# Kernel optimization log

Measured on AMD Instinct MI355X. Metric: run time of the kernel, lower is better.

## Reference

```python
import jax, jax.numpy as jnp
import numpy as np

B, S, M_DIM, N_DIM, K_NNZ = 8, 2048, 2048, 2048, 205


def setup_inputs() -> dict:
    key = jax.random.key(0)
    k1, k2, k3, k4 = jax.random.split(key, 4)
    x = jax.random.normal(k1, (B, S, M_DIM), dtype=jnp.float32)
    # CSR structure: K_NNZ unique, sorted column indices per row
    scores = jax.random.uniform(k2, (N_DIM, M_DIM))
    cols = jnp.sort(jnp.argsort(scores, axis=1)[:, :K_NNZ], axis=1)  # [N, K] unique per row
    indices = cols.reshape(-1).astype(jnp.int32)                      # [nnz]
    indptr = (jnp.arange(N_DIM + 1) * K_NNZ).astype(jnp.int32)        # [N+1]
    W_val = jax.random.normal(k3, (N_DIM * K_NNZ,), dtype=jnp.float32) * (1.0 / np.sqrt(M_DIM))
    bias = jax.random.normal(k4, (N_DIM,), dtype=jnp.float32) * 0.01
    return {"x": x, "W_val": W_val, "bias": bias, "indices": indices, "indptr": indptr}


def reference(x, W_val, bias, indices, indptr):
    # SparseLinear.forward: y = x @ W^T + bias, with W stored in CSR
    # (W_val: nnz values, indptr: [N+1] row pointers, indices: [nnz] column ids).
    N = indptr.shape[0] - 1
    M = x.shape[-1]
    nnz = W_val.shape[0]
    # row id of each nonzero, derived from indptr (standard CSR expansion)
    row_ids = jnp.searchsorted(indptr, jnp.arange(nnz, dtype=indptr.dtype), side="right") - 1
    # materialize the sparse weight (CSR columns are unique per row -> set is exact)
    W = jnp.zeros((N, M), dtype=W_val.dtype).at[row_ids, indices].set(W_val)
    return jnp.einsum("bsm,nm->bsn", x, W) + bias
```

## Files before the change

kernel.cpp:

```cpp
#include <hip/hip_runtime.h>
#include <hip/hip_bf16.h>
#include <stdint.h>

#define M_TOT 16384
#define K_TOT 2048
#define N_TOT 2048

#define BM 256
#define BN 256
#define BK 64
#define LDS_HALF (128 * 64)

#define W_BLOCKS 2048
#define CAST_BLOCKS 16384

typedef __attribute__((ext_vector_type(8))) short short8;
typedef __attribute__((ext_vector_type(4))) float float4v;
typedef __attribute__((ext_vector_type(8))) unsigned short ushort8;

__device__ __forceinline__ unsigned short f2bf_rne(float f) {
    union { float f; unsigned u; } a; a.f = f;
    unsigned r = a.u + 0x7FFFu + ((a.u >> 16) & 1u);
    return (unsigned short)(r >> 16);
}

__global__ void prep_kernel(const float* __restrict__ x,
                            const float* __restrict__ val, const int* __restrict__ idx,
                            const int* __restrict__ indptr,
                            unsigned short* __restrict__ xb, unsigned short* __restrict__ Wb) {
    const int b = blockIdx.x;
    if (b < W_BLOCKS) {
        const int n = b;
        unsigned short* row = Wb + (size_t)n * K_TOT;
        ushort8 z = {0, 0, 0, 0, 0, 0, 0, 0};
        ((ushort8*)row)[threadIdx.x] = z;
        __syncthreads();
        const int s = indptr[n], e = indptr[n + 1];
        for (int j = s + (int)threadIdx.x; j < e; j += (int)blockDim.x)
            row[idx[j]] = f2bf_rne(val[j]);
    } else {
        const int i = (b - W_BLOCKS) * 256 + (int)threadIdx.x;
        const float4* xf = (const float4*)x;
        float4 a = xf[2 * i];
        float4 c = xf[2 * i + 1];
        ushort8 o;
        o[0] = f2bf_rne(a.x); o[1] = f2bf_rne(a.y); o[2] = f2bf_rne(a.z); o[3] = f2bf_rne(a.w);
        o[4] = f2bf_rne(c.x); o[5] = f2bf_rne(c.y); o[6] = f2bf_rne(c.z); o[7] = f2bf_rne(c.w);
        ((ushort8*)xb)[i] = o;
    }
}

__global__ __launch_bounds__(512, 2) void gemm_bias_kernel_256(
    const unsigned short* __restrict__ A,
    const unsigned short* __restrict__ Bw,
    const float* __restrict__ bias,
    float* __restrict__ C)
{
    extern __shared__ unsigned short lds[];

    const int tid  = threadIdx.x;
    const int lane = tid & 63;
    const int wave = tid >> 6;

    const int raw = blockIdx.x;
    const int lid = (raw & 7) * 64 + (raw >> 3);
    const int bm = lid >> 3;
    const int bn = lid & 7;

    const int wrow = wave >> 2;
    const int wcol = wave & 3;
    const int wr16 = wrow * 16;
    const int wc16 = wcol * 16;
    const int mrow = lane & 15;
    const int quad = lane >> 4;
    const int rx   = mrow & 7;

    const int srow = lane >> 3;
    const int csrc = ((lane & 7) ^ srow) * 8;
    const unsigned short* pA = A  + (size_t)(bm * BM + wave * 8 + srow) * K_TOT + csrc;
    const unsigned short* pB = Bw + (size_t)(bn * BN + wave * 8 + srow) * K_TOT + csrc;
    unsigned short* lw = lds + wave * 8 * 64;

    float4v acc[8][4] = {};

#define STAGE(PG, MATIDX, BUF, H, K0)                                            \
    { _Pragma("unroll")                                                          \
      for (int l = 0; l < 2; ++l) {                                              \
        const unsigned short* g = (PG) + ((size_t)((H) * 128 + l * 64) * K_TOT + (size_t)(K0)); \
        unsigned short* lp = lw + (((BUF) * 4 + (MATIDX) * 2 + (H)) * LDS_HALF) + l * 64 * 64;  \
        __builtin_amdgcn_global_load_lds(                                        \
            (const __attribute__((address_space(1))) unsigned int*)g,            \
            (__attribute__((address_space(3))) unsigned int*)lp, 16, 0, 0);      \
      } }

#define WAITV4 asm volatile("s_waitcnt vmcnt(4)" ::: "memory")
#define WAITV0 asm volatile("s_waitcnt vmcnt(0)" ::: "memory")
#define NOSTG  ((void)0)
#define NOWT   ((void)0)

#define PHASE(BUF, MH, NH, STG, TAILW)                                           \
  {                                                                              \
    const unsigned short* Ah = lds + ((BUF) * 4 + (MH)) * LDS_HALF;              \
    const unsigned short* Bh = lds + ((BUF) * 4 + 2 + (NH)) * LDS_HALF;          \
    short8 af[4][2], bfr[2][2];                                                  \
    _Pragma("unroll")                                                            \
    for (int mi = 0; mi < 4; ++mi) {                                             \
      const int r = mi * 32 + wr16 + mrow;                                       \
      _Pragma("unroll")                                                          \
      for (int ks = 0; ks < 2; ++ks)                                             \
        af[mi][ks] = *(const short8*)(Ah + r * 64 + (((ks * 4 + quad) ^ rx) * 8)); \
    }                                                                            \
    _Pragma("unroll")                                                            \
    for (int ni = 0; ni < 2; ++ni) {                                             \
      const int r = ni * 64 + wc16 + mrow;                                       \
      _Pragma("unroll")                                                          \
      for (int ks = 0; ks < 2; ++ks)                                             \
        bfr[ni][ks] = *(const short8*)(Bh + r * 64 + (((ks * 4 + quad) ^ rx) * 8)); \
    }                                                                            \
    STG;                                                                         \
    asm volatile("" ::: "memory");                                               \
    __builtin_amdgcn_s_barrier();                                                \
    asm volatile("s_waitcnt lgkmcnt(0)" ::: "memory");                           \
    __builtin_amdgcn_s_setprio(1);                                               \
    _Pragma("unroll")                                                            \
    for (int mi = 0; mi < 4; ++mi)                                               \
      _Pragma("unroll")                                                          \
      for (int ni = 0; ni < 2; ++ni)                                             \
        _Pragma("unroll")                                                        \
        for (int ks = 0; ks < 2; ++ks)                                           \
          acc[(MH) * 4 + mi][(NH) * 2 + ni] =                                    \
              __builtin_amdgcn_mfma_f32_16x16x32_bf16(                           \
                  af[mi][ks], bfr[ni][ks], acc[(MH) * 4 + mi][(NH) * 2 + ni], 0, 0, 0); \
    __builtin_amdgcn_s_setprio(0);                                               \
    TAILW;                                                                       \
    asm volatile("" ::: "memory");                                               \
    __builtin_amdgcn_s_barrier();                                                \
    asm volatile("" ::: "memory");                                               \
  }

    STAGE(pA, 0, 0, 0, 0);
    STAGE(pB, 1, 0, 1, 0);
    STAGE(pB, 1, 0, 0, 0);
    STAGE(pA, 0, 0, 1, 0);
    STAGE(pA, 0, 1, 0, 64);
    STAGE(pB, 1, 1, 1, 64);
    WAITV4;
    asm volatile("" ::: "memory");
    __builtin_amdgcn_s_barrier();
    asm volatile("" ::: "memory");

    int k0b = 64, k0c = 128, k0d = 192;
#pragma unroll 1
    for (int it = 0; it < 15; ++it) {
        PHASE(0, 0, 0, STAGE(pB, 1, 1, 0, k0b), NOWT)
        PHASE(0, 0, 1, STAGE(pA, 0, 1, 1, k0b), NOWT)
        PHASE(0, 1, 1, STAGE(pA, 0, 0, 0, k0c), NOWT)
        PHASE(0, 1, 0, STAGE(pB, 1, 0, 1, k0c), WAITV4)
        PHASE(1, 0, 0, STAGE(pB, 1, 0, 0, k0c), NOWT)
        PHASE(1, 0, 1, STAGE(pA, 0, 0, 1, k0c), NOWT)
        PHASE(1, 1, 1, STAGE(pA, 0, 1, 0, k0d), NOWT)
        PHASE(1, 1, 0, STAGE(pB, 1, 1, 1, k0d), WAITV4)
        k0b += 128; k0c += 128; k0d += 128;
    }
    PHASE(0, 0, 0, STAGE(pB, 1, 1, 0, k0b), NOWT)
    PHASE(0, 0, 1, STAGE(pA, 0, 1, 1, k0b), NOWT)
    PHASE(0, 1, 1, NOSTG, NOWT)
    PHASE(0, 1, 0, NOSTG, WAITV0)
    PHASE(1, 0, 0, NOSTG, NOWT)
    PHASE(1, 0, 1, NOSTG, NOWT)
    PHASE(1, 1, 1, NOSTG, NOWT)
    PHASE(1, 1, 0, NOSTG, NOWT)

#pragma unroll
    for (int nh = 0; nh < 2; ++nh)
#pragma unroll
        for (int ni = 0; ni < 2; ++ni) {
            const int col = bn * BN + nh * 128 + ni * 64 + wc16 + mrow;
            const float bv = bias[col];
#pragma unroll
            for (int mh = 0; mh < 2; ++mh)
#pragma unroll
                for (int mi = 0; mi < 4; ++mi) {
                    const int row0 = bm * BM + mh * 128 + mi * 32 + wr16 + quad * 4;
#pragma unroll
                    for (int r = 0; r < 4; ++r)
                        C[(size_t)(row0 + r) * N_TOT + col] =
                            acc[mh * 4 + mi][nh * 2 + ni][r] + bv;
                }
        }
#undef PHASE
#undef STAGE
#undef WAITV4
#undef WAITV0
#undef NOSTG
#undef NOWT
}

#define FBM 128
#define FBN 128
#define FBK 64
__global__ __launch_bounds__(256) void gemm_bias_kernel_128(
    const unsigned short* __restrict__ A,
    const unsigned short* __restrict__ Bw,
    const float* __restrict__ bias,
    float* __restrict__ C)
{
    __shared__ unsigned short Asm[FBM * FBK];
    __shared__ unsigned short Bsm[FBN * FBK];

    const int tid  = threadIdx.x;
    const int lane = tid & 63;
    const int wave = tid >> 6;
    const int bm = blockIdx.y;
    const int bn = blockIdx.x;

    const int srow_l = lane >> 3;
    const int schunk = ((lane & 7) ^ srow_l) * 8;
    const unsigned short* a_g[4];
    const unsigned short* b_g[4];
    unsigned short* a_l[4];
    unsigned short* b_l[4];
#pragma unroll
    for (int l = 0; l < 4; ++l) {
        const int row = wave * 32 + l * 8 + srow_l;
        a_g[l] = A  + (size_t)(bm * FBM + row) * K_TOT + schunk;
        b_g[l] = Bw + (size_t)(bn * FBN + row) * K_TOT + schunk;
        a_l[l] = Asm + (wave * 32 + l * 8) * FBK;
        b_l[l] = Bsm + (wave * 32 + l * 8) * FBK;
    }

    const int wm = (wave >> 1) * 64;
    const int wn = (wave & 1) * 64;
    const int mrow = lane & 15;
    const int quad = lane >> 4;
    const int rx   = mrow & 7;

    float4v acc[4][4] = {};

    for (int k0 = 0; k0 < K_TOT; k0 += FBK) {
        __syncthreads();
#pragma unroll
        for (int l = 0; l < 4; ++l)
            __builtin_amdgcn_global_load_lds(
                (const __attribute__((address_space(1))) unsigned int*)(a_g[l] + k0),
                (__attribute__((address_space(3))) unsigned int*)a_l[l], 16, 0, 0);
#pragma unroll
        for (int l = 0; l < 4; ++l)
            __builtin_amdgcn_global_load_lds(
                (const __attribute__((address_space(1))) unsigned int*)(b_g[l] + k0),
                (__attribute__((address_space(3))) unsigned int*)b_l[l], 16, 0, 0);
        __syncthreads();

#pragma unroll
        for (int ks = 0; ks < 2; ++ks) {
            short8 af[4], bf_[4];
#pragma unroll
            for (int mi = 0; mi < 4; ++mi) {
                const int r = wm + mi * 16 + mrow;
                const int slot = (ks * 4 + quad) ^ rx;
                af[mi] = *(const short8*)(Asm + r * FBK + slot * 8);
            }
#pragma unroll
            for (int ni = 0; ni < 4; ++ni) {
                const int r = wn + ni * 16 + mrow;
                const int slot = (ks * 4 + quad) ^ rx;
                bf_[ni] = *(const short8*)(Bsm + r * FBK + slot * 8);
            }
#pragma unroll
            for (int mi = 0; mi < 4; ++mi)
#pragma unroll
                for (int ni = 0; ni < 4; ++ni)
                    acc[mi][ni] = __builtin_amdgcn_mfma_f32_16x16x32_bf16(
                        af[mi], bf_[ni], acc[mi][ni], 0, 0, 0);
        }
    }

#pragma unroll
    for (int ni = 0; ni < 4; ++ni) {
        const int col = bn * FBN + wn + ni * 16 + mrow;
        const float bv = bias[col];
#pragma unroll
        for (int mi = 0; mi < 4; ++mi) {
#pragma unroll
            for (int r = 0; r < 4; ++r) {
                const int row = bm * FBM + wm + mi * 16 + quad * 4 + r;
                C[(size_t)row * N_TOT + col] = acc[mi][ni][r] + bv;
            }
        }
    }
}

extern "C" void kernel_launch(void* const* d_in, const int* in_sizes, int n_in,
                              void* d_out, int out_size, void* d_ws, size_t ws_size,
                              hipStream_t stream) {
    const float* x       = (const float*)d_in[0];
    const float* W_val   = (const float*)d_in[1];
    const float* bias    = (const float*)d_in[2];
    const int*   indices = (const int*)d_in[3];
    const int*   indptr  = (const int*)d_in[4];
    float* out = (float*)d_out;

    unsigned short* xb = (unsigned short*)d_ws;
    unsigned short* Wb = xb + (size_t)M_TOT * K_TOT;
    if (ws_size < ((size_t)M_TOT * K_TOT + (size_t)N_TOT * K_TOT) * sizeof(unsigned short))
        return;

    hipError_t attr_ok = hipFuncSetAttribute(
        reinterpret_cast<const void*>(gemm_bias_kernel_256),
        hipFuncAttributeMaxDynamicSharedMemorySize, 131072);

    prep_kernel<<<W_BLOCKS + CAST_BLOCKS, 256, 0, stream>>>(x, W_val, indices, indptr, xb, Wb);

    if (attr_ok == hipSuccess) {
        gemm_bias_kernel_256<<<dim3(512), 512, 131072, stream>>>(xb, Wb, bias, out);
    } else {
        dim3 grid(N_TOT / FBN, M_TOT / FBM);
        gemm_bias_kernel_128<<<grid, 256, 0, stream>>>(xb, Wb, bias, out);
    }
}
```

Baseline: 355.6 us.

## Reuse LDS fragments across GEMM phases and split prep into cast and densify kernels

The GEMM main loop now keeps the A and B register fragments across phases and reloads only the operand half that changes, using a serpentine phase order, so fewer LDS reads are issued per K step. The combined prep kernel is split into a grid-stride fp32-to-bf16 cast kernel with 4-wide stores and a separate densify kernel. This adds one kernel launch, and the fragments now persist across barriers, which raises register pressure under the 512x2 launch bounds.

```diff
diff --git a/kernel.cpp b/kernel.cpp
--- a/kernel.cpp
+++ b/kernel.cpp
@@ -11,12 +11,10 @@
 #define BK 64
 #define LDS_HALF (128 * 64)
 
-#define W_BLOCKS 2048
-#define CAST_BLOCKS 16384
-
 typedef __attribute__((ext_vector_type(8))) short short8;
 typedef __attribute__((ext_vector_type(4))) float float4v;
 typedef __attribute__((ext_vector_type(8))) unsigned short ushort8;
+typedef __attribute__((ext_vector_type(4))) unsigned short ushort4v;
 
 __device__ __forceinline__ unsigned short f2bf_rne(float f) {
     union { float f; unsigned u; } a; a.f = f;
@@ -24,29 +22,32 @@
     return (unsigned short)(r >> 16);
 }
 
-__global__ void prep_kernel(const float* __restrict__ x,
-                            const float* __restrict__ val, const int* __restrict__ idx,
-                            const int* __restrict__ indptr,
-                            unsigned short* __restrict__ xb, unsigned short* __restrict__ Wb) {
-    const int b = blockIdx.x;
-    if (b < W_BLOCKS) {
-        const int n = b;
-        unsigned short* row = Wb + (size_t)n * K_TOT;
-        ushort8 z = {0, 0, 0, 0, 0, 0, 0, 0};
-        ((ushort8*)row)[threadIdx.x] = z;
-        __syncthreads();
-        const int s = indptr[n], e = indptr[n + 1];
-        for (int j = s + (int)threadIdx.x; j < e; j += (int)blockDim.x)
-            row[idx[j]] = f2bf_rne(val[j]);
-    } else {
-        const int i = (b - W_BLOCKS) * 256 + (int)threadIdx.x;
-        const float4* xf = (const float4*)x;
-        float4 a = xf[2 * i];
-        float4 c = xf[2 * i + 1];
-        ushort8 o;
-        o[0] = f2bf_rne(a.x); o[1] = f2bf_rne(a.y); o[2] = f2bf_rne(a.z); o[3] = f2bf_rne(a.w);
-        o[4] = f2bf_rne(c.x); o[5] = f2bf_rne(c.y); o[6] = f2bf_rne(c.z); o[7] = f2bf_rne(c.w);
-        ((ushort8*)xb)[i] = o;
+__global__ __launch_bounds__(256) void densify_kernel(
+    const float* __restrict__ val, const int* __restrict__ idx,
+    const int* __restrict__ indptr, unsigned short* __restrict__ Wb) {
+    const int n = blockIdx.x;
+    unsigned short* row = Wb + (size_t)n * K_TOT;
+    ushort8 z = {0, 0, 0, 0, 0, 0, 0, 0};
+    ((ushort8*)row)[threadIdx.x] = z;
+    __syncthreads();
+    const int s = indptr[n], e = indptr[n + 1];
+    for (int j = s + (int)threadIdx.x; j < e; j += (int)blockDim.x)
+        row[idx[j]] = f2bf_rne(val[j]);
+}
+
+#define CAST_GRID 2048
+__global__ __launch_bounds__(256) void cast_kernel(
+    const float* __restrict__ x, unsigned short* __restrict__ xb) {
+    const float4* xf = (const float4*)x;
+    size_t i = (size_t)blockIdx.x * 256 + threadIdx.x;
+    const size_t stride = (size_t)CAST_GRID * 256;
+#pragma unroll
+    for (int it = 0; it < 16; ++it, i += stride) {
+        float4 a = xf[i];
+        ushort4v o;
+        o[0] = f2bf_rne(a.x); o[1] = f2bf_rne(a.y);
+        o[2] = f2bf_rne(a.z); o[3] = f2bf_rne(a.w);
+        ((ushort4v*)xb)[i] = o;
     }
 }
 
@@ -82,6 +83,8 @@
     unsigned short* lw = lds + wave * 8 * 64;
 
     float4v acc[8][4] = {};
+    short8 af[4][2];
+    short8 bfr[2][2];
 
 #define STAGE(PG, MATIDX, BUF, H, K0)                                            \
     { _Pragma("unroll")                                                          \
@@ -98,24 +101,27 @@
 #define NOSTG  ((void)0)
 #define NOWT   ((void)0)
 
-#define PHASE(BUF, MH, NH, STG, TAILW)                                           \
+#define PHASE(BUF, MH, NH, DOA, DOB, STG, TAILW)                                 \
   {                                                                              \
-    const unsigned short* Ah = lds + ((BUF) * 4 + (MH)) * LDS_HALF;              \
-    const unsigned short* Bh = lds + ((BUF) * 4 + 2 + (NH)) * LDS_HALF;          \
-    short8 af[4][2], bfr[2][2];                                                  \
-    _Pragma("unroll")                                                            \
-    for (int mi = 0; mi < 4; ++mi) {                                             \
-      const int r = mi * 32 + wr16 + mrow;                                       \
+    if (DOA) {                                                                   \
+      const unsigned short* Ah = lds + ((BUF) * 4 + (MH)) * LDS_HALF;            \
       _Pragma("unroll")                                                          \
-      for (int ks = 0; ks < 2; ++ks)                                             \
-        af[mi][ks] = *(const short8*)(Ah + r * 64 + (((ks * 4 + quad) ^ rx) * 8)); \
+      for (int mi = 0; mi < 4; ++mi) {                                           \
+        const int r = mi * 32 + wr16 + mrow;                                     \
+        _Pragma("unroll")                                                        \
+        for (int ks = 0; ks < 2; ++ks)                                           \
+          af[mi][ks] = *(const short8*)(Ah + r * 64 + (((ks * 4 + quad) ^ rx) * 8)); \
+      }                                                                          \
     }                                                                            \
-    _Pragma("unroll")                                                            \
-    for (int ni = 0; ni < 2; ++ni) {                                             \
-      const int r = ni * 64 + wc16 + mrow;                                       \
+    if (DOB) {                                                                   \
+      const unsigned short* Bh = lds + ((BUF) * 4 + 2 + (NH)) * LDS_HALF;        \
       _Pragma("unroll")                                                          \
-      for (int ks = 0; ks < 2; ++ks)                                             \
-        bfr[ni][ks] = *(const short8*)(Bh + r * 64 + (((ks * 4 + quad) ^ rx) * 8)); \
+      for (int ni = 0; ni < 2; ++ni) {                                           \
+        const int r = ni * 64 + wc16 + mrow;                                     \
+        _Pragma("unroll")                                                        \
+        for (int ks = 0; ks < 2; ++ks)                                           \
+          bfr[ni][ks] = *(const short8*)(Bh + r * 64 + (((ks * 4 + quad) ^ rx) * 8)); \
+      }                                                                          \
     }                                                                            \
     STG;                                                                         \
     asm volatile("" ::: "memory");                                               \
@@ -152,24 +158,24 @@
     int k0b = 64, k0c = 128, k0d = 192;
 #pragma unroll 1
     for (int it = 0; it < 15; ++it) {
-        PHASE(0, 0, 0, STAGE(pB, 1, 1, 0, k0b), NOWT)
-        PHASE(0, 0, 1, STAGE(pA, 0, 1, 1, k0b), NOWT)
-        PHASE(0, 1, 1, STAGE(pA, 0, 0, 0, k0c), NOWT)
-        PHASE(0, 1, 0, STAGE(pB, 1, 0, 1, k0c), WAITV4)
-        PHASE(1, 0, 0, STAGE(pB, 1, 0, 0, k0c), NOWT)
-        PHASE(1, 0, 1, STAGE(pA, 0, 0, 1, k0c), NOWT)
-        PHASE(1, 1, 1, STAGE(pA, 0, 1, 0, k0d), NOWT)
-        PHASE(1, 1, 0, STAGE(pB, 1, 1, 1, k0d), WAITV4)
+        PHASE(0, 0, 0, 1, 1, STAGE(pB, 1, 1, 0, k0b), NOWT)
+        PHASE(0, 0, 1, 0, 1, STAGE(pA, 0, 1, 1, k0b), NOWT)
+        PHASE(0, 1, 1, 1, 0, STAGE(pA, 0, 0, 0, k0c), NOWT)
+        PHASE(0, 1, 0, 0, 1, STAGE(pB, 1, 0, 1, k0c), WAITV4)
+        PHASE(1, 0, 0, 1, 1, STAGE(pB, 1, 0, 0, k0c), NOWT)
+        PHASE(1, 0, 1, 0, 1, STAGE(pA, 0, 0, 1, k0c), NOWT)
+        PHASE(1, 1, 1, 1, 0, STAGE(pA, 0, 1, 0, k0d), NOWT)
+        PHASE(1, 1, 0, 0, 1, STAGE(pB, 1, 1, 1, k0d), WAITV4)
         k0b += 128; k0c += 128; k0d += 128;
     }
-    PHASE(0, 0, 0, STAGE(pB, 1, 1, 0, k0b), NOWT)
-    PHASE(0, 0, 1, STAGE(pA, 0, 1, 1, k0b), NOWT)
-    PHASE(0, 1, 1, NOSTG, NOWT)
-    PHASE(0, 1, 0, NOSTG, WAITV0)
-    PHASE(1, 0, 0, NOSTG, NOWT)
-    PHASE(1, 0, 1, NOSTG, NOWT)
-    PHASE(1, 1, 1, NOSTG, NOWT)
-    PHASE(1, 1, 0, NOSTG, NOWT)
+    PHASE(0, 0, 0, 1, 1, STAGE(pB, 1, 1, 0, k0b), NOWT)
+    PHASE(0, 0, 1, 0, 1, STAGE(pA, 0, 1, 1, k0b), NOWT)
+    PHASE(0, 1, 1, 1, 0, NOSTG, NOWT)
+    PHASE(0, 1, 0, 0, 1, NOSTG, WAITV0)
+    PHASE(1, 0, 0, 1, 1, NOSTG, NOWT)
+    PHASE(1, 0, 1, 0, 1, NOSTG, NOWT)
+    PHASE(1, 1, 1, 1, 0, NOSTG, NOWT)
+    PHASE(1, 1, 0, 0, 1, NOSTG, NOWT)
 
 #pragma unroll
     for (int nh = 0; nh < 2; ++nh)
@@ -309,7 +315,8 @@
         reinterpret_cast<const void*>(gemm_bias_kernel_256),
         hipFuncAttributeMaxDynamicSharedMemorySize, 131072);
 
-    prep_kernel<<<W_BLOCKS + CAST_BLOCKS, 256, 0, stream>>>(x, W_val, indices, indptr, xb, Wb);
+    cast_kernel<<<CAST_GRID, 256, 0, stream>>>(x, xb);
+    densify_kernel<<<N_TOT, 256, 0, stream>>>(W_val, indices, indptr, Wb);
 
     if (attr_ok == hipSuccess) {
         gemm_bias_kernel_256<<<dim3(512), 512, 131072, stream>>>(xb, Wb, bias, out);
```

After: 348.0 us. -2.1%, faster.
